# Kernel tuning notes

Measured on AMD Instinct MI355X. Metric: run time of the kernel, lower is better.

Reference implementation:

```python
import jax, jax.numpy as jnp
import numpy as np

N_WIRES = 12
N_LAYERS = 3
DIM = 2 ** N_WIRES
BATCH = 2048


def _apply_1q(st, g, w):
    # st: (B, 2^n) complex; apply 2x2 gate g on wire w (wire 0 = most significant bit)
    left, right = 2 ** w, 2 ** (N_WIRES - w - 1)
    st = st.reshape(-1, left, 2, right)
    st = jnp.einsum('ij,bljr->blir', g, st)
    return st.reshape(-1, DIM)


def _apply_cnot(st, w):
    # CNOT with control w, target w+1 (adjacent wires)
    left, right = 2 ** w, 2 ** (N_WIRES - w - 2)
    st = st.reshape(-1, left, 2, 2, right)
    st = jnp.stack([st[:, :, 0], st[:, :, 1, ::-1]], axis=2)
    return st.reshape(-1, DIM)


def setup_inputs() -> dict:
    key = jax.random.key(0)
    k1, k2, k3, k4 = jax.random.split(key, 4)
    state_batch = jax.random.normal(k1, (BATCH, DIM), jnp.float32)
    params = jax.random.normal(k2, (N_LAYERS, N_WIRES, 3), jnp.float32)
    head_w = jax.random.normal(k3, (1, N_WIRES), jnp.float32) * (1.0 / np.sqrt(N_WIRES))
    head_b = jax.random.normal(k4, (1,), jnp.float32) * 0.01
    return {"state_batch": state_batch, "params": params, "head_w": head_w, "head_b": head_b}


def reference(state_batch, params, head_w, head_b):
    # StatePreparation requires normalized amplitudes
    st = state_batch / jnp.linalg.norm(state_batch, axis=-1, keepdims=True)
    st = st.astype(jnp.complex64)
    for layer in range(N_LAYERS):
        for w in range(N_WIRES):
            tx, ty, tz = params[layer, w, 0], params[layer, w, 1], params[layer, w, 2]
            cx, sx = jnp.cos(tx / 2), jnp.sin(tx / 2)
            cy, sy = jnp.cos(ty / 2), jnp.sin(ty / 2)
            RX = jnp.array([[cx, -1j * sx], [-1j * sx, cx]])
            RY = jnp.array([[cy, -sy], [sy, cy]]).astype(jnp.complex64)
            ez = jnp.exp(-1j * tz / 2)
            RZ = jnp.array([[ez, 0.0], [0.0, jnp.conj(ez)]])
            # circuit applies RX then RY then RZ -> fused matrix RZ @ RY @ RX
            st = _apply_1q(st, RZ @ RY @ RX, w)
        for w in range(N_WIRES - 1):
            st = _apply_cnot(st, w)
    probs = st.real ** 2 + st.imag ** 2  # (B, 2^n)
    evs = []
    for w in range(N_WIRES):
        pr = probs.reshape(-1, 2 ** w, 2, 2 ** (N_WIRES - w - 1)).sum(axis=(1, 3))
        evs.append(pr[:, 0] - pr[:, 1])  # <Z_w>
    qout = jnp.stack(evs, axis=-1)  # (B, n_wires)
    return (qout @ head_w.T + head_b).squeeze(-1)
```

## Files before the change

### kernel.cpp

```cpp
#include <hip/hip_runtime.h>
#include <math.h>

#define DIM 4096


typedef float f2 __attribute__((ext_vector_type(2)));


__device__ __forceinline__ f2 cfma(f2 acc, f2 c, f2 v) {
  asm("v_pk_fma_f32 %0, %1, %2, %0 op_sel:[0,0,0] op_sel_hi:[0,1,1]\n\t"
      "v_pk_fma_f32 %0, %1, %2, %0 op_sel:[1,1,0] op_sel_hi:[1,0,1] neg_lo:[1,0,0]"
      : "+&v"(acc) : "v"(c), "v"(v));
  return acc;
}
__device__ __forceinline__ f2 cfma_cj(f2 acc, f2 c, f2 v) {
  asm("v_pk_fma_f32 %0, %1, %2, %0 op_sel:[0,0,0] op_sel_hi:[0,1,1]\n\t"
      "v_pk_fma_f32 %0, %1, %2, %0 op_sel:[1,1,0] op_sel_hi:[1,0,1] neg_hi:[1,0,0]"
      : "+&v"(acc) : "v"(c), "v"(v));
  return acc;
}
__device__ __forceinline__ f2 cmul(f2 c, f2 v) {
  f2 d;
  asm("v_pk_mul_f32 %0, %1, %2 op_sel:[0,0] op_sel_hi:[0,1]\n\t"
      "v_pk_fma_f32 %0, %1, %2, %0 op_sel:[1,1,0] op_sel_hi:[1,0,1] neg_lo:[1,0,0]"
      : "=&v"(d) : "v"(c), "v"(v));
  return d;
}
__device__ __forceinline__ f2 cmul_ncj(f2 c, f2 v) {
  f2 d;
  asm("v_pk_mul_f32 %0, %1, %2 op_sel:[0,0] op_sel_hi:[0,1] neg_lo:[1,0] neg_hi:[1,0]\n\t"
      "v_pk_fma_f32 %0, %1, %2, %0 op_sel:[1,1,0] op_sel_hi:[1,0,1] neg_lo:[1,0,0]"
      : "=&v"(d) : "v"(c), "v"(v));
  return d;
}

__device__ __forceinline__ int h4(int x) {
  return (x ^ (x >> 1) ^ (x >> 2) ^ (x >> 3)) & 15;
}

template<int M>
__device__ __forceinline__ float xch(float x, int paddr) {
  int xi = __float_as_int(x);
  if constexpr (M == 1) {
    return __int_as_float(__builtin_amdgcn_mov_dpp(xi, 0xB1, 0xF, 0xF, false));
  } else if constexpr (M == 2) {
    return __int_as_float(__builtin_amdgcn_mov_dpp(xi, 0x4E, 0xF, 0xF, false));
  } else if constexpr (M == 4) {
    int r = __builtin_amdgcn_update_dpp(xi, xi, 0x104, 0xF, 0x5, false);
    r     = __builtin_amdgcn_update_dpp(r,  xi, 0x114, 0xF, 0xA, false);
    return __int_as_float(r);
  } else if constexpr (M == 8) {
    return __int_as_float(__builtin_amdgcn_mov_dpp(xi, 0x128, 0xF, 0xF, false));
  } else if constexpr (M == 16) {
    return __int_as_float(__builtin_amdgcn_ds_swizzle(xi, 0x401F));
  } else {
    return __int_as_float(__builtin_amdgcn_ds_bpermute(paddr, xi));
  }
}

template<int M>
__device__ __forceinline__ void lane_gate(float4 g, int t, int paddr,
                                          f2* __restrict__ z) {
  const bool hi = (t & M) != 0;
  const float sgn = hi ? -1.f : 1.f;
  const f2 c1 = { g.x, sgn * g.y };
  const f2 c2 = { sgn * g.z, g.w };
  #pragma unroll
  for (int p = 0; p < 16; ++p) {
    f2 pp;
    pp.x = xch<M>(z[p].x, paddr);
    pp.y = xch<M>(z[p].y, paddr);
    z[p] = cfma(cmul(c1, z[p]), c2, pp);
  }
}

__global__ __launch_bounds__(256)
void qsim_kernel(const float* __restrict__ in, const float* __restrict__ params,
                 const float* __restrict__ hw, const float* __restrict__ hb,
                 float* __restrict__ out) {
  __shared__ f2 st2[DIM];
  __shared__ float4 ga4[36];
  __shared__ float red[4];

  const int t = threadIdx.x;
  const int b = blockIdx.x;

  if (t < 36) {
    const float* P = params + t * 3;
    float hx = P[0]*0.5f, hy = P[1]*0.5f, hz = P[2]*0.5f;
    float cx = cosf(hx), sx = sinf(hx);
    float cy = cosf(hy), sy = sinf(hy);
    float cz = cosf(hz), sz = sinf(hz);
    float arr = cy*cx, aii = sy*sx, brr = sy*cx, bii = cy*sx;
    ga4[t] = make_float4(cz*arr + sz*aii,
                         cz*aii - sz*arr,
                         -(cz*brr + sz*bii),
                         -(cz*bii - sz*brr));
  }

  float ld[16];
  const float* inb = in + (size_t)b * DIM + t * 16;
  float ss = 0.f;
  #pragma unroll
  for (int q = 0; q < 4; ++q) {
    float4 v = reinterpret_cast<const float4*>(inb)[q];
    ld[4*q+0]=v.x; ld[4*q+1]=v.y; ld[4*q+2]=v.z; ld[4*q+3]=v.w;
    ss += v.x*v.x + v.y*v.y + v.z*v.z + v.w*v.w;
  }
  #pragma unroll
  for (int o = 1; o < 64; o <<= 1) ss += __shfl_xor(ss, o, 64);
  if ((t & 63) == 0) red[t >> 6] = ss;
  __syncthreads();
  float inv = 1.0f / sqrtf(red[0] + red[1] + red[2] + red[3]);
  f2 z[16];
  #pragma unroll
  for (int j = 0; j < 16; ++j) z[j] = (f2){ ld[j] * inv, 0.f };

  const int wbase = (t << 4) ^ h4(t & 15);
  const int sig   = (t << 4) ^ (t << 3);
  const int sigc  = sig & 1023;
  const int gb    = sigc ^ h4((sigc >> 4) & 15);
  const int x11   = (t >> 7) & 1;
  const int x10   = ((t >> 6) ^ (t >> 7)) & 1;
  const int paddr = ((t ^ 32) & 63) << 2;

  #pragma unroll 1
  for (int L = 0; L < 3; ++L) {
    #pragma unroll
    for (int w = 8; w <= 11; ++w) {
      const int m = 1 << (11 - w);
      float4 g = ga4[L*12 + w];
      const f2 a  = { g.x, g.y };
      const f2 bb = { g.z, g.w };
      #pragma unroll
      for (int p = 0; p < 16; ++p) {
        if (!(p & m)) {
          const int k2 = p | m;
          f2 v0 = z[p], v1 = z[k2];
          z[p]  = cfma(cmul(a, v0), bb, v1);
          z[k2] = cfma_cj(cmul_ncj(bb, v0), a, v1);
        }
      }
    }
    lane_gate<32>(ga4[L*12 + 2], t, paddr, z);
    lane_gate<16>(ga4[L*12 + 3], t, paddr, z);
    lane_gate< 8>(ga4[L*12 + 4], t, paddr, z);
    lane_gate< 4>(ga4[L*12 + 5], t, paddr, z);
    lane_gate< 2>(ga4[L*12 + 6], t, paddr, z);
    lane_gate< 1>(ga4[L*12 + 7], t, paddr, z);

    #pragma unroll
    for (int j = 0; j < 16; ++j) st2[wbase ^ j] = z[j];
    __syncthreads();

    float4 g0 = ga4[L*12 + 0], g1 = ga4[L*12 + 1];
    float u0r, u0i, u1r, u1i, v0r, v0i, v1r, v1i;
    if (x11) { u0r = -g0.z; u0i = g0.w; u1r = g0.x; u1i = -g0.y; }
    else     { u0r =  g0.x; u0i = g0.y; u1r = g0.z; u1i =  g0.w; }
    if (x10) { v0r = -g1.z; v0i = g1.w; v1r = g1.x; v1i = -g1.y; }
    else     { v0r =  g1.x; v0i = g1.y; v1r = g1.z; v1i =  g1.w; }
    const f2 c0 = { u0r*v0r - u0i*v0i, u0r*v0i + u0i*v0r };
    const f2 c1 = { u0r*v1r - u0i*v1i, u0r*v1i + u0i*v1r };
    const f2 c2 = { u1r*v0r - u1i*v0i, u1r*v0i + u1i*v0r };
    const f2 c3 = { u1r*v1r - u1i*v1i, u1r*v1i + u1i*v1r };
    #pragma unroll
    for (int j = 0; j < 16; ++j) {
      const int base = gb ^ (j ^ (j >> 1));
      f2 m0 = st2[base];
      f2 m1 = st2[base + 1024];
      f2 m2 = st2[base + 2048];
      f2 m3 = st2[base + 3072];
      z[j] = cfma(cfma(cfma(cmul(c0, m0), c1, m1), c2, m2), c3, m3);
    }
    if (L != 2) __syncthreads();
  }

  float Ct = 0.f;
  #pragma unroll
  for (int p = 0; p < 8; ++p) Ct += hw[7-p] * (((t >> p) & 1) ? -1.f : 1.f);
  float h11 = hw[11], h10 = hw[10], h9 = hw[9], h8 = hw[8];
  float acc = 0.f;
  #pragma unroll
  for (int j = 0; j < 16; ++j) {
    float pj = z[j].x*z[j].x + z[j].y*z[j].y;
    float cj = Ct + ((j&1) ? -h11 : h11) + ((j&2) ? -h10 : h10)
             + ((j&4) ? -h9  : h9 ) + ((j&8) ? -h8  : h8 );
    acc += pj * cj;
  }
  #pragma unroll
  for (int o = 1; o < 64; o <<= 1) acc += __shfl_xor(acc, o, 64);
  if ((t & 63) == 0) red[t >> 6] = acc;
  __syncthreads();
  if (t == 0) out[b] = red[0] + red[1] + red[2] + red[3] + hb[0];
}

extern "C" void kernel_launch(void* const* d_in, const int* in_sizes, int n_in,
                              void* d_out, int out_size, void* d_ws, size_t ws_size,
                              hipStream_t stream) {
  const float* st     = (const float*)d_in[0];
  const float* params = (const float*)d_in[1];
  const float* hwp    = (const float*)d_in[2];
  const float* hbp    = (const float*)d_in[3];
  float* outp = (float*)d_out;
  int batch = in_sizes[0] / DIM;
  qsim_kernel<<<batch, 256, 0, stream>>>(st, params, hwp, hbp, outp);
}
```

Baseline: 64.14 us.

## Split each state across 512 threads with 8 amplitudes per thread

Each block now uses 512 threads that hold 8 amplitudes each instead of 256 threads holding 16. The work per thread is repartitioned: three wires are handled in registers, six across lanes, and three through shared memory with an 8-term fused gate. This lowers register pressure and is meant to raise occupancy and parallelism. In exchange, each thread does more shared-memory reads per amplitude, the block reductions grow to 8 entries, and the index mapping has to be rederived.

```diff
diff --git a/kernel.cpp b/kernel.cpp
--- a/kernel.cpp
+++ b/kernel.cpp
@@ -5,7 +5,6 @@
 
 
 typedef float f2 __attribute__((ext_vector_type(2)));
-
 
 __device__ __forceinline__ f2 cfma(f2 acc, f2 c, f2 v) {
   asm("v_pk_fma_f32 %0, %1, %2, %0 op_sel:[0,0,0] op_sel_hi:[0,1,1]\n\t"
@@ -66,7 +65,7 @@
   const f2 c1 = { g.x, sgn * g.y };
   const f2 c2 = { sgn * g.z, g.w };
   #pragma unroll
-  for (int p = 0; p < 16; ++p) {
+  for (int p = 0; p < 8; ++p) {
     f2 pp;
     pp.x = xch<M>(z[p].x, paddr);
     pp.y = xch<M>(z[p].y, paddr);
@@ -74,13 +73,13 @@
   }
 }
 
-__global__ __launch_bounds__(256)
+__global__ __launch_bounds__(512)
 void qsim_kernel(const float* __restrict__ in, const float* __restrict__ params,
                  const float* __restrict__ hw, const float* __restrict__ hb,
                  float* __restrict__ out) {
   __shared__ f2 st2[DIM];
   __shared__ float4 ga4[36];
-  __shared__ float red[4];
+  __shared__ float red[8];
 
   const int t = threadIdx.x;
   const int b = blockIdx.x;
@@ -98,11 +97,11 @@
                          -(cz*bii - sz*brr));
   }
 
-  float ld[16];
-  const float* inb = in + (size_t)b * DIM + t * 16;
+  float ld[8];
+  const float* inb = in + (size_t)b * DIM + t * 8;
   float ss = 0.f;
   #pragma unroll
-  for (int q = 0; q < 4; ++q) {
+  for (int q = 0; q < 2; ++q) {
     float4 v = reinterpret_cast<const float4*>(inb)[q];
     ld[4*q+0]=v.x; ld[4*q+1]=v.y; ld[4*q+2]=v.z; ld[4*q+3]=v.w;
     ss += v.x*v.x + v.y*v.y + v.z*v.z + v.w*v.w;
@@ -111,29 +110,30 @@
   for (int o = 1; o < 64; o <<= 1) ss += __shfl_xor(ss, o, 64);
   if ((t & 63) == 0) red[t >> 6] = ss;
   __syncthreads();
-  float inv = 1.0f / sqrtf(red[0] + red[1] + red[2] + red[3]);
-  f2 z[16];
-  #pragma unroll
-  for (int j = 0; j < 16; ++j) z[j] = (f2){ ld[j] * inv, 0.f };
-
-  const int wbase = (t << 4) ^ h4(t & 15);
-  const int sig   = (t << 4) ^ (t << 3);
-  const int sigc  = sig & 1023;
+  float inv = 1.0f / sqrtf(red[0]+red[1]+red[2]+red[3]+red[4]+red[5]+red[6]+red[7]);
+  f2 z[8];
+  #pragma unroll
+  for (int j = 0; j < 8; ++j) z[j] = (f2){ ld[j] * inv, 0.f };
+
+  const int wbase = (t << 3) ^ h4((t >> 1) & 15);
+  const int sig0  = (t << 3) ^ (t << 2);
+  const int sigc  = sig0 & 511;
   const int gb    = sigc ^ h4((sigc >> 4) & 15);
-  const int x11   = (t >> 7) & 1;
-  const int x10   = ((t >> 6) ^ (t >> 7)) & 1;
+  const int x11   = (t >> 8) & 1;
+  const int x10   = ((t >> 7) ^ (t >> 8)) & 1;
+  const int x9    = ((t >> 6) ^ (t >> 7)) & 1;
   const int paddr = ((t ^ 32) & 63) << 2;
 
   #pragma unroll 1
   for (int L = 0; L < 3; ++L) {
     #pragma unroll
-    for (int w = 8; w <= 11; ++w) {
+    for (int w = 9; w <= 11; ++w) {
       const int m = 1 << (11 - w);
       float4 g = ga4[L*12 + w];
       const f2 a  = { g.x, g.y };
       const f2 bb = { g.z, g.w };
       #pragma unroll
-      for (int p = 0; p < 16; ++p) {
+      for (int p = 0; p < 8; ++p) {
         if (!(p & m)) {
           const int k2 = p | m;
           f2 v0 = z[p], v1 = z[k2];
@@ -142,56 +142,67 @@
         }
       }
     }
-    lane_gate<32>(ga4[L*12 + 2], t, paddr, z);
-    lane_gate<16>(ga4[L*12 + 3], t, paddr, z);
-    lane_gate< 8>(ga4[L*12 + 4], t, paddr, z);
-    lane_gate< 4>(ga4[L*12 + 5], t, paddr, z);
-    lane_gate< 2>(ga4[L*12 + 6], t, paddr, z);
-    lane_gate< 1>(ga4[L*12 + 7], t, paddr, z);
+    lane_gate<32>(ga4[L*12 + 3], t, paddr, z);
+    lane_gate<16>(ga4[L*12 + 4], t, paddr, z);
+    lane_gate< 8>(ga4[L*12 + 5], t, paddr, z);
+    lane_gate< 4>(ga4[L*12 + 6], t, paddr, z);
+    lane_gate< 2>(ga4[L*12 + 7], t, paddr, z);
+    lane_gate< 1>(ga4[L*12 + 8], t, paddr, z);
 
     #pragma unroll
-    for (int j = 0; j < 16; ++j) st2[wbase ^ j] = z[j];
+    for (int j = 0; j < 8; ++j) st2[wbase ^ j] = z[j];
     __syncthreads();
 
-    float4 g0 = ga4[L*12 + 0], g1 = ga4[L*12 + 1];
-    float u0r, u0i, u1r, u1i, v0r, v0i, v1r, v1i;
-    if (x11) { u0r = -g0.z; u0i = g0.w; u1r = g0.x; u1i = -g0.y; }
-    else     { u0r =  g0.x; u0i = g0.y; u1r = g0.z; u1i =  g0.w; }
-    if (x10) { v0r = -g1.z; v0i = g1.w; v1r = g1.x; v1i = -g1.y; }
-    else     { v0r =  g1.x; v0i = g1.y; v1r = g1.z; v1i =  g1.w; }
-    const f2 c0 = { u0r*v0r - u0i*v0i, u0r*v0i + u0i*v0r };
-    const f2 c1 = { u0r*v1r - u0i*v1i, u0r*v1i + u0i*v1r };
-    const f2 c2 = { u1r*v0r - u1i*v0i, u1r*v0i + u1i*v0r };
-    const f2 c3 = { u1r*v1r - u1i*v1i, u1r*v1i + u1i*v1r };
+    float4 g0 = ga4[L*12 + 0], g1 = ga4[L*12 + 1], g2 = ga4[L*12 + 2];
+    f2 U0, U1, V0, V1, W0, W1;
+    if (x11) { U0 = (f2){-g0.z, g0.w}; U1 = (f2){g0.x, -g0.y}; }
+    else     { U0 = (f2){ g0.x, g0.y}; U1 = (f2){g0.z,  g0.w}; }
+    if (x10) { V0 = (f2){-g1.z, g1.w}; V1 = (f2){g1.x, -g1.y}; }
+    else     { V0 = (f2){ g1.x, g1.y}; V1 = (f2){g1.z,  g1.w}; }
+    if (x9)  { W0 = (f2){-g2.z, g2.w}; W1 = (f2){g2.x, -g2.y}; }
+    else     { W0 = (f2){ g2.x, g2.y}; W1 = (f2){g2.z,  g2.w}; }
+    f2 uv00 = cmul(U0, V0), uv01 = cmul(U0, V1);
+    f2 uv10 = cmul(U1, V0), uv11 = cmul(U1, V1);
+    f2 c0 = cmul(uv00, W0), c1 = cmul(uv00, W1);
+    f2 c2 = cmul(uv01, W0), c3 = cmul(uv01, W1);
+    f2 c4 = cmul(uv10, W0), c5 = cmul(uv10, W1);
+    f2 c6 = cmul(uv11, W0), c7 = cmul(uv11, W1);
     #pragma unroll
-    for (int j = 0; j < 16; ++j) {
+    for (int j = 0; j < 8; ++j) {
       const int base = gb ^ (j ^ (j >> 1));
       f2 m0 = st2[base];
-      f2 m1 = st2[base + 1024];
-      f2 m2 = st2[base + 2048];
-      f2 m3 = st2[base + 3072];
-      z[j] = cfma(cfma(cfma(cmul(c0, m0), c1, m1), c2, m2), c3, m3);
+      f2 m1 = st2[base +  512];
+      f2 m2 = st2[base + 1024];
+      f2 m3 = st2[base + 1536];
+      f2 m4 = st2[base + 2048];
+      f2 m5 = st2[base + 2560];
+      f2 m6 = st2[base + 3072];
+      f2 m7 = st2[base + 3584];
+      f2 a1 = cfma(cfma(cfma(cmul(c0, m0), c1, m1), c2, m2), c3, m3);
+      f2 a2 = cfma(cfma(cfma(cmul(c4, m4), c5, m5), c6, m6), c7, m7);
+      z[j] = a1 + a2;
     }
     if (L != 2) __syncthreads();
   }
 
   float Ct = 0.f;
   #pragma unroll
-  for (int p = 0; p < 8; ++p) Ct += hw[7-p] * (((t >> p) & 1) ? -1.f : 1.f);
-  float h11 = hw[11], h10 = hw[10], h9 = hw[9], h8 = hw[8];
+  for (int p = 0; p < 9; ++p) Ct += hw[8-p] * (((t >> p) & 1) ? -1.f : 1.f);
+  float h9 = hw[9], h10 = hw[10], h11 = hw[11];
   float acc = 0.f;
   #pragma unroll
-  for (int j = 0; j < 16; ++j) {
+  for (int j = 0; j < 8; ++j) {
     float pj = z[j].x*z[j].x + z[j].y*z[j].y;
-    float cj = Ct + ((j&1) ? -h11 : h11) + ((j&2) ? -h10 : h10)
-             + ((j&4) ? -h9  : h9 ) + ((j&8) ? -h8  : h8 );
+    float cj = Ct + ((j&4) ? -h9 : h9) + ((j&2) ? -h10 : h10)
+             + ((j&1) ? -h11 : h11);
     acc += pj * cj;
   }
   #pragma unroll
   for (int o = 1; o < 64; o <<= 1) acc += __shfl_xor(acc, o, 64);
   if ((t & 63) == 0) red[t >> 6] = acc;
   __syncthreads();
-  if (t == 0) out[b] = red[0] + red[1] + red[2] + red[3] + hb[0];
+  if (t == 0)
+    out[b] = red[0]+red[1]+red[2]+red[3]+red[4]+red[5]+red[6]+red[7] + hb[0];
 }
 
 extern "C" void kernel_launch(void* const* d_in, const int* in_sizes, int n_in,
@@ -203,5 +214,5 @@
   const float* hbp    = (const float*)d_in[3];
   float* outp = (float*)d_out;
   int batch = in_sizes[0] / DIM;
-  qsim_kernel<<<batch, 256, 0, stream>>>(st, params, hwp, hbp, outp);
-}
+  qsim_kernel<<<batch, 512, 0, stream>>>(st, params, hwp, hbp, outp);
+}
```

Result: slower. 73.34 us (+14.3%).
